# Optimization experiments

Hardware: AMD Instinct MI355X
Metric: run time of the kernel (lower is better)

Reference implementation:

```python
import jax, jax.numpy as jnp
import numpy as np

B, L, S, H = 2, 256, 384, 768
Tc, Dc = 16, 50
WV, WD = 20000, 100
CV = 128
NEG = -1e30


def _lstm_scan(x, Wih, Whh, bih, bhh):
    # x: [N, T, D] -> hs: [N, T, Hc]; torch LSTM gate order i,f,g,o
    N = x.shape[0]
    Hc = Whh.shape[1]
    h0 = jnp.zeros((N, Hc), x.dtype)

    def step(carry, xt):
        h, c = carry
        g = xt @ Wih.T + h @ Whh.T + bih + bhh  # [N, 4Hc]
        i, f, gg, o = jnp.split(g, 4, axis=-1)
        i = jax.nn.sigmoid(i)
        f = jax.nn.sigmoid(f)
        gg = jnp.tanh(gg)
        o = jax.nn.sigmoid(o)
        c = f * c + i * gg
        h = o * jnp.tanh(c)
        return (h, c), h

    _, hs = jax.lax.scan(step, (h0, h0), jnp.swapaxes(x, 0, 1))
    return jnp.swapaxes(hs, 0, 1)


def setup_inputs() -> dict:
    key = jax.random.key(0)
    ks = jax.random.split(key, 10)
    bert_emb = jax.random.normal(ks[0], (B, S, H), jnp.float32)
    pieces2word = jax.random.randint(ks[1], (B, L, S), 0, 2, jnp.int32)
    word_ids = jax.random.randint(ks[2], (B, L), 0, WV, jnp.int32)
    char_count = jax.random.randint(ks[3], (B, L), 1, Tc + 1, jnp.int32)
    char_ids = jax.random.randint(ks[4], (B, L, Tc), 0, CV, jnp.int32)
    # mask consistent with ragged char lengths (first char_count positions valid)
    token_masks_char = (jnp.arange(Tc)[None, None, :] < char_count[..., None]).astype(jnp.int32)
    word_table = jax.random.normal(ks[5], (WV, WD), jnp.float32) * 0.02
    char_table = jax.random.normal(ks[6], (CV, Dc), jnp.float32) * 0.02
    sc = 1.0 / np.sqrt(Dc)

    def lstm_w(k):
        a, b, c, d = jax.random.split(k, 4)
        return (jax.random.uniform(a, (4 * Dc, Dc), jnp.float32, -sc, sc),
                jax.random.uniform(b, (4 * Dc, Dc), jnp.float32, -sc, sc),
                jax.random.uniform(c, (4 * Dc,), jnp.float32, -sc, sc),
                jax.random.uniform(d, (4 * Dc,), jnp.float32, -sc, sc))

    Wih_f, Whh_f, bih_f, bhh_f = lstm_w(ks[7])
    Wih_b, Whh_b, bih_b, bhh_b = lstm_w(ks[8])
    return dict(bert_emb=bert_emb, pieces2word=pieces2word, word_ids=word_ids,
                char_count=char_count, char_ids=char_ids, token_masks_char=token_masks_char,
                word_table=word_table, char_table=char_table,
                Wih_f=Wih_f, Whh_f=Whh_f, bih_f=bih_f, bhh_f=bhh_f,
                Wih_b=Wih_b, Whh_b=Whh_b, bih_b=bih_b, bhh_b=bhh_b)


def reference(bert_emb, pieces2word, word_ids, char_count, char_ids, token_masks_char,
              word_table, char_table, Wih_f, Whh_f, bih_f, bhh_f, Wih_b, Whh_b, bih_b, bhh_b):
    # --- piece2word max pool (expand + masked_fill(min) + max over pieces) ---
    minv = jnp.min(bert_emb)
    # [B, L, S, H] intermediate, as in the original expand
    masked = jnp.where(pieces2word[..., None] != 0, bert_emb[:, None, :, :], minv)
    word_reps = jnp.max(masked, axis=2)  # [B, L, H]
    # dropouts are identity in eval mode

    # --- word embedding lookup ---
    word_embed = word_table[word_ids]  # [B, L, WD]

    # --- char bi-LSTM with packed-sequence semantics ---
    lens = jnp.maximum(char_count.reshape(-1), 1)  # char_count[char_count==0]=1
    x = char_table[char_ids.reshape(B * L, Tc)]  # [N, Tc, Dc]
    h_fwd = _lstm_scan(x, Wih_f, Whh_f, bih_f, bhh_f)
    # reverse each sequence within its valid length for the backward direction
    t = jnp.arange(Tc)[None, :]
    idx = jnp.where(t < lens[:, None], lens[:, None] - 1 - t, t)  # [N, Tc]
    x_rev = jnp.take_along_axis(x, idx[..., None], axis=1)
    h_bwd = _lstm_scan(x_rev, Wih_b, Whh_b, bih_b, bhh_b)
    h_bwd = jnp.take_along_axis(h_bwd, idx[..., None], axis=1)  # back to original order
    h = jnp.concatenate([h_fwd, h_bwd], axis=-1)  # [N, Tc, 2*Dc]
    valid = (t < lens[:, None])[..., None]
    h = jnp.where(valid, h, 0.0)  # pad_packed_sequence zero-pads beyond length
    h = h.reshape(B, L, Tc, 2 * Dc)

    # --- combine(..., 'max'): masked max over ragged char groups ---
    m = jnp.where(token_masks_char[..., None] == 0, NEG, 0.0)
    sup = jnp.max(m + h, axis=2)  # [B, L, 2*Dc]
    sup = jnp.where(sup == NEG, 0.0, sup)

    return jnp.concatenate([word_reps, word_embed, sup], axis=-1)  # [B, L, H+WD+2*Dc]
```

## Files before the change

kernel.cpp:

```cpp
#include <hip/hip_runtime.h>
#include <float.h>

#define Bb 2
#define Ll 256
#define Ss 384
#define Hh 768
#define Tc 16
#define Dc 50
#define WD 100
#define CV 128
#define NG 200
#define OUTC 968


__device__ inline float tanh_fast(float x) {
    float e = __expf(2.f * x);
    return 1.f - 2.f / (e + 1.f);
}
__device__ inline float sigmoid_fast(float x) {
    return 1.f / (1.f + __expf(-x));
}


__global__ __launch_bounds__(256) void kernel1(
        const float* __restrict__ bert, const float* __restrict__ char_table,
        const float* __restrict__ Wih_f, const float* __restrict__ bih_f, const float* __restrict__ bhh_f,
        const float* __restrict__ Wih_b, const float* __restrict__ bih_b, const float* __restrict__ bhh_b,
        float* __restrict__ minp, float* __restrict__ xpt) {
    int blk = blockIdx.x, tid = threadIdx.x;
    if (blk < 128) {
        const int n4 = (Bb * Ss * Hh) / 4;
        const float4* b4 = (const float4*)bert;
        float m = FLT_MAX;
        for (int i = blk * 256 + tid; i < n4; i += 128 * 256) {
            float4 v = b4[i];
            m = fminf(m, fminf(fminf(v.x, v.y), fminf(v.z, v.w)));
        }
        #pragma unroll
        for (int off = 32; off; off >>= 1) m = fminf(m, __shfl_down(m, off, 64));
        __shared__ float red[4];
        if ((tid & 63) == 0) red[tid >> 6] = m;
        __syncthreads();
        if (tid == 0) minp[blk] = fminf(fminf(red[0], red[1]), fminf(red[2], red[3]));
    } else {
        int idx = blk - 128;
        int dir = idx >> 3, c0 = (idx & 7) * 16;
        const float* Wih = dir ? Wih_b : Wih_f;
        const float* bih = dir ? bih_b : bih_f;
        const float* bhh = dir ? bhh_b : bhh_f;
        __shared__ float ct[16][Dc];
        for (int e = tid; e < 16 * Dc; e += 256)
            ((float*)ct)[e] = char_table[c0 * Dc + e];
        __syncthreads();
        if (tid < NG) {
            float w[Dc];
            #pragma unroll
            for (int j = 0; j < Dc; j++) w[j] = Wih[tid * Dc + j];
            float bias = bih[tid] + bhh[tid];
            for (int cid = 0; cid < 16; cid++) {
                float a = bias;
                #pragma unroll
                for (int j = 0; j < Dc; j++) a += w[j] * ct[cid][j];
                xpt[(dir * CV + c0 + cid) * NG + tid] = a;
            }
        }
    }
}


__global__ __launch_bounds__(256, 4) void kernel_lstm(
        const int* __restrict__ char_ids, const int* __restrict__ char_count,
        const float* __restrict__ Whh_f, const float* __restrict__ Whh_b,
        const float* __restrict__ xpt, float* __restrict__ out) {
    __shared__ __align__(16) float xg[Tc][NG];
    __shared__ __align__(16) float gsb[2][NG];
    __shared__ int scid[Tc];

    int blk = blockIdx.x, tid = threadIdx.x;
    int n = blk >> 1, dir = blk & 1;
    const float* Whh = dir ? Whh_b : Whh_f;
    int lane = tid & 63;

    int len = char_count[n];
    if (len < 1) len = 1;
    if (tid < Tc) {
        int st = dir ? (tid < len ? len - 1 - tid : tid) : tid;
        scid[tid] = char_ids[n * Tc + st];
    }
    __syncthreads();

    for (int e = tid; e < Tc * (NG / 4); e += 256) {
        int t = e / 50, q = e - t * 50;
        ((float4*)xg[t])[q] = ((const float4*)&xpt[(dir * CV + scid[t]) * NG])[q];
    }
    int wrow = tid < NG ? tid : NG - 1;
    bool istanh = (tid >= 100 && tid < 150);
    float w[50];
    #pragma unroll
    for (int j = 0; j < 50; j++) w[j] = Whh[wrow * 50 + j];
    __syncthreads();

    int ch = lane < 50 ? lane : 49;
    float c = 0.f, h = 0.f, maxv = -FLT_MAX;
    for (int t = 0; t < Tc; t++) {
        int hb = __float_as_int(h);
        float g0 = xg[t][wrow], g1 = 0.f, g2 = 0.f, g3 = 0.f;
        #pragma unroll
        for (int j = 0; j < 48; j += 4) {
            g0 = fmaf(__int_as_float(__builtin_amdgcn_readlane(hb, j)),     w[j],     g0);
            g1 = fmaf(__int_as_float(__builtin_amdgcn_readlane(hb, j + 1)), w[j + 1], g1);
            g2 = fmaf(__int_as_float(__builtin_amdgcn_readlane(hb, j + 2)), w[j + 2], g2);
            g3 = fmaf(__int_as_float(__builtin_amdgcn_readlane(hb, j + 3)), w[j + 3], g3);
        }
        g0 = fmaf(__int_as_float(__builtin_amdgcn_readlane(hb, 48)), w[48], g0);
        g1 = fmaf(__int_as_float(__builtin_amdgcn_readlane(hb, 49)), w[49], g1);
        float g = (g0 + g1) + (g2 + g3);
        if (tid < NG)
            gsb[t & 1][tid] = istanh ? tanh_fast(g) : sigmoid_fast(g);
        __syncthreads();
        float si = gsb[t & 1][ch];
        float sf = gsb[t & 1][ch + 50];
        float tg = gsb[t & 1][ch + 100];
        float so = gsb[t & 1][ch + 150];
        c = sf * c + si * tg;
        h = so * tanh_fast(c);
        if (t < len) maxv = fmaxf(maxv, h);
    }
    if (tid < 50)
        out[(size_t)n * OUTC + (Hh + WD) + dir * Dc + tid] = maxv;
}


__global__ __launch_bounds__(256) void kernel_word(
        const float* __restrict__ bert, const int* __restrict__ p2w,
        const float* __restrict__ minp,
        const int* __restrict__ word_ids, const float* __restrict__ word_table,
        float* __restrict__ out) {
    __shared__ __align__(16) float sm[Ss][4];
    __shared__ __align__(16) float sacc[4][4][128];
    __shared__ float sminv;
    int blk = blockIdx.x, tid = threadIdx.x;

    if (blk < 768) {
        int hc  = blk % 6;
        int lt  = (blk / 6) & 63;
        int b   = blk / 384;
        int l0  = lt * 4;

        const int* pm = p2w + ((size_t)(b * Ll + l0)) * Ss;
        for (int e = tid; e < 4 * Ss; e += 256) {
            int r = e / Ss, s = e - r * Ss;
            sm[s][r] = pm[r * Ss + s] ? 0.f : -FLT_MAX;
        }
        if (tid < 64) {
            float m = fminf(minp[tid], minp[tid + 64]);
            #pragma unroll
            for (int off = 32; off; off >>= 1) m = fminf(m, __shfl_down(m, off, 64));
            if (tid == 0) sminv = m;
        }
        __syncthreads();

        int w    = tid >> 6;
        int lane = tid & 63;
        int s0 = w * 96;

        const float2* bb2 = (const float2*)(bert + (size_t)b * Ss * Hh) + hc * 64 + lane;
        float2 acc[4];
        #pragma unroll
        for (int r = 0; r < 4; r++) { acc[r].x = -FLT_MAX; acc[r].y = -FLT_MAX; }

        for (int jo = 0; jo < 96; jo += 8) {
            float2 v[8];
            #pragma unroll
            for (int k = 0; k < 8; k++) v[k] = bb2[(size_t)(s0 + jo + k) * 384];
            #pragma unroll
            for (int k = 0; k < 8; k++) {
                int j = s0 + jo + k;
                float4 q = *(const float4*)&sm[j][0];
                acc[0].x = fmaxf(acc[0].x, v[k].x + q.x);
                acc[0].y = fmaxf(acc[0].y, v[k].y + q.x);
                acc[1].x = fmaxf(acc[1].x, v[k].x + q.y);
                acc[1].y = fmaxf(acc[1].y, v[k].y + q.y);
                acc[2].x = fmaxf(acc[2].x, v[k].x + q.z);
                acc[2].y = fmaxf(acc[2].y, v[k].y + q.z);
                acc[3].x = fmaxf(acc[3].x, v[k].x + q.w);
                acc[3].y = fmaxf(acc[3].y, v[k].y + q.w);
            }
        }
        #pragma unroll
        for (int r = 0; r < 4; r++)
            *(float2*)&sacc[w][r][lane * 2] = acc[r];
        __syncthreads();

        float mv = sminv;
        for (int e = tid; e < 4 * 128; e += 256) {
            int r = e >> 7, cx = e & 127;
            float m = fmaxf(fmaxf(sacc[0][r][cx], sacc[1][r][cx]),
                            fmaxf(sacc[2][r][cx], sacc[3][r][cx]));
            if (m == -FLT_MAX) m = mv;
            out[((size_t)(b * Ll + l0 + r)) * OUTC + hc * 128 + cx] = m;
        }
    } else {
        for (int i = (blk - 768) * 256 + tid; i < Bb * Ll * WD; i += 64 * 256) {
            int bl = i / WD, d = i - bl * WD;
            out[(size_t)bl * OUTC + Hh + d] = word_table[(size_t)word_ids[bl] * WD + d];
        }
    }
}

extern "C" void kernel_launch(void* const* d_in, const int* in_sizes, int n_in,
                              void* d_out, int out_size, void* d_ws, size_t ws_size,
                              hipStream_t stream) {
    const float* bert       = (const float*)d_in[0];
    const int*   p2w        = (const int*)d_in[1];
    const int*   word_ids   = (const int*)d_in[2];
    const int*   char_count = (const int*)d_in[3];
    const int*   char_ids   = (const int*)d_in[4];
    const float* word_table = (const float*)d_in[6];
    const float* char_table = (const float*)d_in[7];
    const float* Wih_f = (const float*)d_in[8];
    const float* Whh_f = (const float*)d_in[9];
    const float* bih_f = (const float*)d_in[10];
    const float* bhh_f = (const float*)d_in[11];
    const float* Wih_b = (const float*)d_in[12];
    const float* Whh_b = (const float*)d_in[13];
    const float* bih_b = (const float*)d_in[14];
    const float* bhh_b = (const float*)d_in[15];
    float* out = (float*)d_out;

    float* minp = (float*)d_ws;
    float* xpt  = minp + 128;

    kernel1<<<144, 256, 0, stream>>>(
        bert, char_table, Wih_f, bih_f, bhh_f, Wih_b, bih_b, bhh_b,
        minp, xpt);
    kernel_lstm<<<1024, 256, 0, stream>>>(
        char_ids, char_count, Whh_f, Whh_b, xpt, out);
    kernel_word<<<832, 256, 0, stream>>>(
        bert, p2w, minp, word_ids, word_table, out);
}
```

Before: 129.9 us.

## Merge LSTM and word-pooling kernels into one interleaved launch with 8-row tiles

Fuses the char-LSTM kernel and the word max-pooling/embedding kernel into a single launch whose blocks are assigned roles, interleaving one pooling block with two LSTM blocks so latency-bound LSTM work overlaps bandwidth-bound pooling. The pooling tile grows from 4 to 8 words per block, doubling reuse of each loaded bert row and halving the number of pooling blocks. This removes one kernel launch and its tail, at the cost of a larger shared-memory footprint, more registers from a shared union-style smem layout, and possible occupancy limits for the LSTM role under the combined register budget.

Result: faster. 123.9 us (-4.6%).

```diff
diff --git a/kernel.cpp b/kernel.cpp
--- a/kernel.cpp
+++ b/kernel.cpp
@@ -68,87 +68,93 @@
 }
 
 
-__global__ __launch_bounds__(256, 4) void kernel_lstm(
+__global__ __launch_bounds__(256, 4) void kernel2(
         const int* __restrict__ char_ids, const int* __restrict__ char_count,
         const float* __restrict__ Whh_f, const float* __restrict__ Whh_b,
-        const float* __restrict__ xpt, float* __restrict__ out) {
-    __shared__ __align__(16) float xg[Tc][NG];
-    __shared__ __align__(16) float gsb[2][NG];
-    __shared__ int scid[Tc];
-
-    int blk = blockIdx.x, tid = threadIdx.x;
-    int n = blk >> 1, dir = blk & 1;
-    const float* Whh = dir ? Whh_b : Whh_f;
-    int lane = tid & 63;
-
-    int len = char_count[n];
-    if (len < 1) len = 1;
-    if (tid < Tc) {
-        int st = dir ? (tid < len ? len - 1 - tid : tid) : tid;
-        scid[tid] = char_ids[n * Tc + st];
-    }
-    __syncthreads();
-
-    for (int e = tid; e < Tc * (NG / 4); e += 256) {
-        int t = e / 50, q = e - t * 50;
-        ((float4*)xg[t])[q] = ((const float4*)&xpt[(dir * CV + scid[t]) * NG])[q];
-    }
-    int wrow = tid < NG ? tid : NG - 1;
-    bool istanh = (tid >= 100 && tid < 150);
-    float w[50];
-    #pragma unroll
-    for (int j = 0; j < 50; j++) w[j] = Whh[wrow * 50 + j];
-    __syncthreads();
-
-    int ch = lane < 50 ? lane : 49;
-    float c = 0.f, h = 0.f, maxv = -FLT_MAX;
-    for (int t = 0; t < Tc; t++) {
-        int hb = __float_as_int(h);
-        float g0 = xg[t][wrow], g1 = 0.f, g2 = 0.f, g3 = 0.f;
-        #pragma unroll
-        for (int j = 0; j < 48; j += 4) {
-            g0 = fmaf(__int_as_float(__builtin_amdgcn_readlane(hb, j)),     w[j],     g0);
-            g1 = fmaf(__int_as_float(__builtin_amdgcn_readlane(hb, j + 1)), w[j + 1], g1);
-            g2 = fmaf(__int_as_float(__builtin_amdgcn_readlane(hb, j + 2)), w[j + 2], g2);
-            g3 = fmaf(__int_as_float(__builtin_amdgcn_readlane(hb, j + 3)), w[j + 3], g3);
-        }
-        g0 = fmaf(__int_as_float(__builtin_amdgcn_readlane(hb, 48)), w[48], g0);
-        g1 = fmaf(__int_as_float(__builtin_amdgcn_readlane(hb, 49)), w[49], g1);
-        float g = (g0 + g1) + (g2 + g3);
-        if (tid < NG)
-            gsb[t & 1][tid] = istanh ? tanh_fast(g) : sigmoid_fast(g);
-        __syncthreads();
-        float si = gsb[t & 1][ch];
-        float sf = gsb[t & 1][ch + 50];
-        float tg = gsb[t & 1][ch + 100];
-        float so = gsb[t & 1][ch + 150];
-        c = sf * c + si * tg;
-        h = so * tanh_fast(c);
-        if (t < len) maxv = fmaxf(maxv, h);
-    }
-    if (tid < 50)
-        out[(size_t)n * OUTC + (Hh + WD) + dir * Dc + tid] = maxv;
-}
-
-
-__global__ __launch_bounds__(256) void kernel_word(
+        const float* __restrict__ xpt,
         const float* __restrict__ bert, const int* __restrict__ p2w,
         const float* __restrict__ minp,
         const int* __restrict__ word_ids, const float* __restrict__ word_table,
         float* __restrict__ out) {
-    __shared__ __align__(16) float sm[Ss][4];
-    __shared__ __align__(16) float sacc[4][4][128];
-    __shared__ float sminv;
+    __shared__ __align__(16) char smem[28680];
     int blk = blockIdx.x, tid = threadIdx.x;
 
-    if (blk < 768) {
-        int hc  = blk % 6;
-        int lt  = (blk / 6) & 63;
-        int b   = blk / 384;
-        int l0  = lt * 4;
+    int role, id;
+    if (blk < 1152) {
+        int g = blk / 3, r3 = blk - g * 3;
+        role = r3 == 0 ? 0 : 1;
+        id = r3 == 0 ? g : g * 2 + (r3 - 1);
+    } else if (blk < 1408) { role = 1; id = 768 + (blk - 1152); }
+    else { role = 2; id = blk - 1408; }
+
+    if (role == 1) {
+        float (*xg)[NG] = (float (*)[NG])smem;
+        float (*gsb)[NG] = (float (*)[NG])(smem + 12800);
+        int*   scid = (int*)(smem + 14400);
+
+        int n = id >> 1, dir = id & 1;
+        const float* Whh = dir ? Whh_b : Whh_f;
+        int lane = tid & 63;
+
+        int len = char_count[n];
+        if (len < 1) len = 1;
+        if (tid < Tc) {
+            int st = dir ? (tid < len ? len - 1 - tid : tid) : tid;
+            scid[tid] = char_ids[n * Tc + st];
+        }
+        __syncthreads();
+
+        for (int e = tid; e < Tc * (NG / 4); e += 256) {
+            int t = e / 50, q = e - t * 50;
+            ((float4*)xg[t])[q] = ((const float4*)&xpt[(dir * CV + scid[t]) * NG])[q];
+        }
+        int wrow = tid < NG ? tid : NG - 1;
+        bool istanh = (tid >= 100 && tid < 150);
+        float w[50];
+        #pragma unroll
+        for (int j = 0; j < 50; j++) w[j] = Whh[wrow * 50 + j];
+        __syncthreads();
+
+        int ch = lane < 50 ? lane : 49;
+        float c = 0.f, h = 0.f, maxv = -FLT_MAX;
+        for (int t = 0; t < Tc; t++) {
+            int hb = __float_as_int(h);
+            float g0 = xg[t][wrow], g1 = 0.f, g2 = 0.f, g3 = 0.f;
+            #pragma unroll
+            for (int j = 0; j < 48; j += 4) {
+                g0 = fmaf(__int_as_float(__builtin_amdgcn_readlane(hb, j)),     w[j],     g0);
+                g1 = fmaf(__int_as_float(__builtin_amdgcn_readlane(hb, j + 1)), w[j + 1], g1);
+                g2 = fmaf(__int_as_float(__builtin_amdgcn_readlane(hb, j + 2)), w[j + 2], g2);
+                g3 = fmaf(__int_as_float(__builtin_amdgcn_readlane(hb, j + 3)), w[j + 3], g3);
+            }
+            g0 = fmaf(__int_as_float(__builtin_amdgcn_readlane(hb, 48)), w[48], g0);
+            g1 = fmaf(__int_as_float(__builtin_amdgcn_readlane(hb, 49)), w[49], g1);
+            float g = (g0 + g1) + (g2 + g3);
+            if (tid < NG)
+                gsb[t & 1][tid] = istanh ? tanh_fast(g) : sigmoid_fast(g);
+            __syncthreads();
+            float si = gsb[t & 1][ch];
+            float sf = gsb[t & 1][ch + 50];
+            float tg = gsb[t & 1][ch + 100];
+            float so = gsb[t & 1][ch + 150];
+            c = sf * c + si * tg;
+            h = so * tanh_fast(c);
+            if (t < len) maxv = fmaxf(maxv, h);
+        }
+        if (tid < 50)
+            out[(size_t)n * OUTC + (Hh + WD) + dir * Dc + tid] = maxv;
+    } else if (role == 0) {
+        float (*sm)[8] = (float (*)[8])smem;
+        float (*sacc)[8][128] = (float (*)[8][128])(smem + 12288);
+        float* sminv = (float*)(smem + 28672);
+
+        int hc  = id % 6;
+        int lt  = (id / 6) & 31;
+        int b   = id / 192;
+        int l0  = lt * 8;
 
         const int* pm = p2w + ((size_t)(b * Ll + l0)) * Ss;
-        for (int e = tid; e < 4 * Ss; e += 256) {
+        for (int e = tid; e < 8 * Ss; e += 256) {
             int r = e / Ss, s = e - r * Ss;
             sm[s][r] = pm[r * Ss + s] ? 0.f : -FLT_MAX;
         }
@@ -156,7 +162,7 @@
             float m = fminf(minp[tid], minp[tid + 64]);
             #pragma unroll
             for (int off = 32; off; off >>= 1) m = fminf(m, __shfl_down(m, off, 64));
-            if (tid == 0) sminv = m;
+            if (tid == 0) *sminv = m;
         }
         __syncthreads();
 
@@ -165,9 +171,9 @@
         int s0 = w * 96;
 
         const float2* bb2 = (const float2*)(bert + (size_t)b * Ss * Hh) + hc * 64 + lane;
-        float2 acc[4];
-        #pragma unroll
-        for (int r = 0; r < 4; r++) { acc[r].x = -FLT_MAX; acc[r].y = -FLT_MAX; }
+        float2 acc[8];
+        #pragma unroll
+        for (int r = 0; r < 8; r++) { acc[r].x = -FLT_MAX; acc[r].y = -FLT_MAX; }
 
         for (int jo = 0; jo < 96; jo += 8) {
             float2 v[8];
@@ -176,24 +182,33 @@
             #pragma unroll
             for (int k = 0; k < 8; k++) {
                 int j = s0 + jo + k;
-                float4 q = *(const float4*)&sm[j][0];
-                acc[0].x = fmaxf(acc[0].x, v[k].x + q.x);
-                acc[0].y = fmaxf(acc[0].y, v[k].y + q.x);
-                acc[1].x = fmaxf(acc[1].x, v[k].x + q.y);
-                acc[1].y = fmaxf(acc[1].y, v[k].y + q.y);
-                acc[2].x = fmaxf(acc[2].x, v[k].x + q.z);
-                acc[2].y = fmaxf(acc[2].y, v[k].y + q.z);
-                acc[3].x = fmaxf(acc[3].x, v[k].x + q.w);
-                acc[3].y = fmaxf(acc[3].y, v[k].y + q.w);
+                float4 q0 = *(const float4*)&sm[j][0];
+                float4 q1 = *(const float4*)&sm[j][4];
+                acc[0].x = fmaxf(acc[0].x, v[k].x + q0.x);
+                acc[0].y = fmaxf(acc[0].y, v[k].y + q0.x);
+                acc[1].x = fmaxf(acc[1].x, v[k].x + q0.y);
+                acc[1].y = fmaxf(acc[1].y, v[k].y + q0.y);
+                acc[2].x = fmaxf(acc[2].x, v[k].x + q0.z);
+                acc[2].y = fmaxf(acc[2].y, v[k].y + q0.z);
+                acc[3].x = fmaxf(acc[3].x, v[k].x + q0.w);
+                acc[3].y = fmaxf(acc[3].y, v[k].y + q0.w);
+                acc[4].x = fmaxf(acc[4].x, v[k].x + q1.x);
+                acc[4].y = fmaxf(acc[4].y, v[k].y + q1.x);
+                acc[5].x = fmaxf(acc[5].x, v[k].x + q1.y);
+                acc[5].y = fmaxf(acc[5].y, v[k].y + q1.y);
+                acc[6].x = fmaxf(acc[6].x, v[k].x + q1.z);
+                acc[6].y = fmaxf(acc[6].y, v[k].y + q1.z);
+                acc[7].x = fmaxf(acc[7].x, v[k].x + q1.w);
+                acc[7].y = fmaxf(acc[7].y, v[k].y + q1.w);
             }
         }
         #pragma unroll
-        for (int r = 0; r < 4; r++)
+        for (int r = 0; r < 8; r++)
             *(float2*)&sacc[w][r][lane * 2] = acc[r];
         __syncthreads();
 
-        float mv = sminv;
-        for (int e = tid; e < 4 * 128; e += 256) {
+        float mv = *sminv;
+        for (int e = tid; e < 8 * 128; e += 256) {
             int r = e >> 7, cx = e & 127;
             float m = fmaxf(fmaxf(sacc[0][r][cx], sacc[1][r][cx]),
                             fmaxf(sacc[2][r][cx], sacc[3][r][cx]));
@@ -201,7 +216,7 @@
             out[((size_t)(b * Ll + l0 + r)) * OUTC + hc * 128 + cx] = m;
         }
     } else {
-        for (int i = (blk - 768) * 256 + tid; i < Bb * Ll * WD; i += 64 * 256) {
+        for (int i = id * 256 + tid; i < Bb * Ll * WD; i += 64 * 256) {
             int bl = i / WD, d = i - bl * WD;
             out[(size_t)bl * OUTC + Hh + d] = word_table[(size_t)word_ids[bl] * WD + d];
         }
@@ -234,8 +249,7 @@
     kernel1<<<144, 256, 0, stream>>>(
         bert, char_table, Wih_f, bih_f, bhh_f, Wih_b, bih_b, bhh_b,
         minp, xpt);
-    kernel_lstm<<<1024, 256, 0, stream>>>(
-        char_ids, char_count, Whh_f, Whh_b, xpt, out);
-    kernel_word<<<832, 256, 0, stream>>>(
-        bert, p2w, minp, word_ids, word_table, out);
-}
+    kernel2<<<1472, 256, 0, stream>>>(
+        char_ids, char_count, Whh_f, Whh_b, xpt, bert, p2w, minp,
+        word_ids, word_table, out);
+}
```
